# Kernel tuning notes

Hardware: AMD Instinct MI355X
Metric: run time of the kernel (lower is better)

Reference implementation:

```python
import jax, jax.numpy as jnp
import numpy as np

D = 2048      # feature dim (fc1 = Linear(2*2048, 2048))
S = 10240


def setup_inputs() -> dict:
    key = jax.random.key(0)
    ks = jax.random.split(key, 16)
    sc = 0.02
    z = lambda *s: jnp.zeros(s, jnp.float32)
    return {
        "x0": jax.random.normal(ks[0], (1, 1, D), jnp.float32),
        "x1": jax.random.normal(ks[1], (1, S, D), jnp.float32),
        # fc1: Linear(4096, 2048)  (stored input-major for x @ W)
        "W1": jax.random.normal(ks[2], (2 * D, D), jnp.float32) * sc,
        "b1": z(D),
        # fc2: Linear(2048, 1)
        "W2": jax.random.normal(ks[3], (D, 1), jnp.float32) * sc,
        "b2": z(1),
        # LSTM(input=1, hidden=1, bidirectional): per-direction gate params [4] = (i,f,g,o)
        "Wih_f": jax.random.normal(ks[4], (4,), jnp.float32) * 0.5,
        "Whh_f": jax.random.normal(ks[5], (4,), jnp.float32) * 0.5,
        "bih_f": z(4),
        "bhh_f": z(4),
        "Wih_b": jax.random.normal(ks[6], (4,), jnp.float32) * 0.5,
        "Whh_b": jax.random.normal(ks[7], (4,), jnp.float32) * 0.5,
        "bih_b": z(4),
        "bhh_b": z(4),
        # fc3: Linear(10, 1)
        "W3": jax.random.normal(ks[8], (10, 1), jnp.float32) * sc,
        "b3": z(1),
    }


def _lstm_dir(x_seq, Wih, Whh, bih, bhh):
    """Single-direction LSTM, input_size=hidden_size=1, batch=1.
    x_seq: [S] scalars. Returns h sequence [S]. PyTorch gate order (i,f,g,o)."""
    b = bih + bhh

    def step(carry, x):
        h, c = carry
        g = Wih * x + Whh * h + b              # [4]
        i = jax.nn.sigmoid(g[0])
        f = jax.nn.sigmoid(g[1])
        gg = jnp.tanh(g[2])
        o = jax.nn.sigmoid(g[3])
        c = f * c + i * gg
        h = o * jnp.tanh(c)
        return (h, c), h

    h0 = jnp.zeros((), x_seq.dtype)
    c0 = jnp.zeros((), x_seq.dtype)
    _, hs = jax.lax.scan(step, (h0, c0), x_seq)
    return hs


def reference(x0, x1, W1, b1, W2, b2,
              Wih_f, Whh_f, bih_f, bhh_f,
              Wih_b, Whh_b, bih_b, bhh_b,
              W3, b3):
    # similarity: cat(|x0 - x1|, x0 + x1) along features (x0 broadcasts over S)
    sim = jnp.concatenate([jnp.abs(x0 - x1), x0 + x1], axis=2)   # [1, S, 2D]
    h = jax.nn.relu(jnp.einsum('bsf,fd->bsd', sim, W1) + b1)     # [1, S, D]
    # (dropout is identity in eval mode)
    s = jax.nn.sigmoid(jnp.einsum('bsd,do->bso', h, W2) + b2)    # [1, S, 1]
    x_seq = s[0, :, 0]                                           # [S]

    h_f = _lstm_dir(x_seq, Wih_f, Whh_f, bih_f, bhh_f)           # [S]
    h_b = _lstm_dir(x_seq[::-1], Wih_b, Whh_b, bih_b, bhh_b)[::-1]
    out = jnp.stack([h_f, h_b], axis=1)                          # [S, 2] == lstm out [S,1,2]

    grp = out.reshape(1, -1, 10)                                 # [1, S*2/10, 10]
    y = jax.nn.sigmoid(grp @ W3 + b3)                            # [1, S*2/10, 1]
    return y.reshape(1, -1)
```

## Files before the change

kernel.cpp:

```cpp
#include <hip/hip_runtime.h>
#include <hip/hip_bf16.h>

#define DD 2048
#define SS 10240
#define KK 4096

typedef __bf16 bf16x8 __attribute__((ext_vector_type(8)));
typedef float  f32x4  __attribute__((ext_vector_type(4)));

__device__ __forceinline__ unsigned short f2bf_rne(float x) {
    unsigned int u = __float_as_uint(x);
    u += 0x7FFFu + ((u >> 16) & 1u);
    return (unsigned short)(u >> 16);
}

__global__ __launch_bounds__(256) void prep_sim_kernel(
    const float* __restrict__ W1, const float* __restrict__ b2,
    const float* __restrict__ x0, const float* __restrict__ x1,
    unsigned short* __restrict__ W1T, float* __restrict__ s_pre,
    unsigned short* __restrict__ simB) {
    __shared__ float tile[64][65];
    const int t = threadIdx.x;

    if (blockIdx.x < (KK / 64) * (DD / 64)) {
        const int bf = blockIdx.x % (KK / 64);
        const int bd = blockIdx.x / (KK / 64);
        const int f0 = bf * 64, d0 = bd * 64;
#pragma unroll
        for (int p = 0; p < 4; ++p) {
            int fr = p * 16 + (t >> 4);
            int dc = (t & 15) * 4;
            const float4 v = *(const float4*)&W1[(size_t)(f0 + fr) * DD + d0 + dc];
            tile[fr][dc + 0] = v.x; tile[fr][dc + 1] = v.y;
            tile[fr][dc + 2] = v.z; tile[fr][dc + 3] = v.w;
        }
        __syncthreads();
#pragma unroll
        for (int p = 0; p < 4; ++p) {
            int dr = p * 16 + (t >> 4);
            int fc = (t & 15) * 4;
            ushort4 o;
            o.x = f2bf_rne(tile[fc + 0][dr]);
            o.y = f2bf_rne(tile[fc + 1][dr]);
            o.z = f2bf_rne(tile[fc + 2][dr]);
            o.w = f2bf_rne(tile[fc + 3][dr]);
            *(ushort4*)&W1T[(size_t)(d0 + dr) * KK + f0 + fc] = o;
        }
        int gid = blockIdx.x * 256 + t;
        if (gid < SS) s_pre[gid] = b2[0];
    } else {
        const int s = blockIdx.x - (KK / 64) * (DD / 64);
        const int d = t * 8;
        const float4 a0 = *(const float4*)&x0[d];
        const float4 a1 = *(const float4*)&x0[d + 4];
        const float4 v0 = *(const float4*)&x1[(size_t)s * DD + d];
        const float4 v1 = *(const float4*)&x1[(size_t)s * DD + d + 4];
        ushort4 lo0, lo1, hi0, hi1;
        lo0.x = f2bf_rne(fabsf(a0.x - v0.x)); hi0.x = f2bf_rne(a0.x + v0.x);
        lo0.y = f2bf_rne(fabsf(a0.y - v0.y)); hi0.y = f2bf_rne(a0.y + v0.y);
        lo0.z = f2bf_rne(fabsf(a0.z - v0.z)); hi0.z = f2bf_rne(a0.z + v0.z);
        lo0.w = f2bf_rne(fabsf(a0.w - v0.w)); hi0.w = f2bf_rne(a0.w + v0.w);
        lo1.x = f2bf_rne(fabsf(a1.x - v1.x)); hi1.x = f2bf_rne(a1.x + v1.x);
        lo1.y = f2bf_rne(fabsf(a1.y - v1.y)); hi1.y = f2bf_rne(a1.y + v1.y);
        lo1.z = f2bf_rne(fabsf(a1.z - v1.z)); hi1.z = f2bf_rne(a1.z + v1.z);
        lo1.w = f2bf_rne(fabsf(a1.w - v1.w)); hi1.w = f2bf_rne(a1.w + v1.w);
        unsigned short* row = &simB[(size_t)s * KK];
        *(ushort4*)&row[d]          = lo0;
        *(ushort4*)&row[d + 4]      = lo1;
        *(ushort4*)&row[DD + d]     = hi0;
        *(ushort4*)&row[DD + d + 4] = hi1;
    }
}

#define BM3 320
#define BN3 256
#define BK3 64
#define NKT (KK / BK3)

#define STAGE_A(ktv, BUFV)                                                     \
    _Pragma("unroll")                                                          \
    for (int L = 0; L < 5; ++L) {                                              \
        __builtin_amdgcn_global_load_lds(                                      \
            (const __attribute__((address_space(1))) void*)(gA + (size_t)L * 64 * KK + (size_t)(ktv) * 64), \
            (__attribute__((address_space(3))) void*)&lds[BUFV][t * 8 + L * 4096], \
            16, 0, 0);                                                         \
    }
#define STAGE_B(ktv, BUFV)                                                     \
    _Pragma("unroll")                                                          \
    for (int L = 0; L < 4; ++L) {                                              \
        __builtin_amdgcn_global_load_lds(                                      \
            (const __attribute__((address_space(1))) void*)(gB + (size_t)L * 64 * KK + (size_t)(ktv) * 64), \
            (__attribute__((address_space(3))) void*)&lds[BUFV][20480 + t * 8 + L * 4096], \
            16, 0, 0);                                                         \
    }

#define BODY(ktv, BUF, SA_LIT, SB_LIT, DO_STAGE)                               \
    {                                                                          \
        asm volatile("s_waitcnt vmcnt(" SA_LIT ")" ::: "memory");              \
        __builtin_amdgcn_s_barrier();                                          \
        __builtin_amdgcn_sched_barrier(0);                                     \
        if (DO_STAGE) { STAGE_A((ktv) + 1, BUF ^ 1) }                          \
        asm volatile("s_waitcnt vmcnt(" SB_LIT ")" ::: "memory");              \
        __builtin_amdgcn_s_barrier();                                          \
        __builtin_amdgcn_sched_barrier(0);                                     \
        if (DO_STAGE) { STAGE_B((ktv) + 1, BUF ^ 1) }                          \
        _Pragma("unroll")                                                      \
        for (int ks = 0; ks < 2; ++ks) {                                       \
            const int gx = ks ? gx1 : gx0;                                     \
            bf16x8 bfr[8];                                                     \
            _Pragma("unroll")                                                  \
            for (int n = 0; n < 8; ++n)                                        \
                bfr[n] = *(const bf16x8*)&lds[BUF][boff + n * 1024 + gx];      \
            _Pragma("unroll")                                                  \
            for (int m = 0; m < 5; ++m) {                                      \
                bf16x8 afr = *(const bf16x8*)&lds[BUF][aoff + m * 1024 + gx];  \
                __builtin_amdgcn_s_setprio(1);                                 \
                _Pragma("unroll")                                              \
                for (int n = 0; n < 8; ++n)                                    \
                    acc[m][n] = __builtin_amdgcn_mfma_f32_16x16x32_bf16(       \
                        afr, bfr[n], acc[m][n], 0, 0, 0);                      \
                __builtin_amdgcn_s_setprio(0);                                 \
            }                                                                  \
        }                                                                      \
    }

__global__ __launch_bounds__(512, 2) void gemm3_kernel(
    const unsigned short* __restrict__ simB,
    const unsigned short* __restrict__ W1T,
    const float* __restrict__ b1, const float* __restrict__ W2,
    float* __restrict__ s_pre) {
    __shared__ unsigned short lds[2][36864];

    const int t    = threadIdx.x;
    const int lane = t & 63;
    const int wv   = t >> 6;
    const int wr   = wv >> 1;
    const int wc   = wv & 1;
    const int lr   = lane & 15;
    const int g4   = lane >> 4;
    const int l7   = lane & 7;

    const int bm = blockIdx.x & 31;
    const int bn = blockIdx.x >> 5;
    const int m0 = bm * BM3, n0 = bn * BN3;

    const int trow = t >> 3;
    const int gsrc = (t & 7) ^ (trow & 7);
    const unsigned short* gA = simB + (size_t)(m0 + trow) * KK + gsrc * 8;
    const unsigned short* gB = W1T  + (size_t)(n0 + trow) * KK + gsrc * 8;

    const int aoff = (wr * 80 + lr) * 64;
    const int boff = 20480 + (wc * 128 + lr) * 64;
    const int gx0  = ((0 * 4 + g4) ^ l7) * 8;
    const int gx1  = ((1 * 4 + g4) ^ l7) * 8;

    f32x4 acc[5][8];
#pragma unroll
    for (int m = 0; m < 5; ++m)
#pragma unroll
        for (int n = 0; n < 8; ++n)
            acc[m][n] = (f32x4){0.f, 0.f, 0.f, 0.f};

    STAGE_A(0, 0)
    STAGE_B(0, 0)

#pragma unroll 1
    for (int kt = 0; kt < NKT - 2; kt += 2) {
        BODY(kt,     0, "4", "5", 1)
        BODY(kt + 1, 1, "4", "5", 1)
    }
    BODY(NKT - 2, 0, "4", "5", 1)
    BODY(NKT - 1, 1, "4", "0", 0)

    float b1v[8], w2v[8];
#pragma unroll
    for (int n = 0; n < 8; ++n) {
        int col = n0 + wc * 128 + n * 16 + lr;
        b1v[n] = b1[col];
        w2v[n] = W2[col];
    }
#pragma unroll
    for (int m = 0; m < 5; ++m) {
#pragma unroll
        for (int r = 0; r < 4; ++r) {
            float rowsum = 0.f;
#pragma unroll
            for (int n = 0; n < 8; ++n) {
                float v = acc[m][n][r] + b1v[n];
                v = fmaxf(v, 0.f);
                rowsum = fmaf(v, w2v[n], rowsum);
            }
            rowsum += __shfl_xor(rowsum, 1);
            rowsum += __shfl_xor(rowsum, 2);
            rowsum += __shfl_xor(rowsum, 4);
            rowsum += __shfl_xor(rowsum, 8);
            if (lr == 0) {
                int row = m0 + wr * 80 + m * 16 + g4 * 4 + r;
                atomicAdd(&s_pre[row], rowsum);
            }
        }
    }
}

#define BM 128
#define BN 128
#define BK 32

__global__ __launch_bounds__(256) void gemm_kernel(
    const float* __restrict__ x0, const float* __restrict__ x1,
    const unsigned short* __restrict__ W1T,
    const float* __restrict__ b1, const float* __restrict__ W2,
    float* __restrict__ s_pre) {
    __shared__ unsigned short As[BM][BK];
    __shared__ unsigned short Bs[BN][BK];

    const int tid  = threadIdx.x;
    const int lane = tid & 63;
    const int wave = tid >> 6;
    const int wr = wave >> 1, wc = wave & 1;
    const int bm = blockIdx.x / (DD / BN);
    const int bn = blockIdx.x % (DD / BN);
    const int m0 = bm * BM, n0 = bn * BN;
    const int lr = lane & 15;
    const int lk = (lane >> 4) * 8;

    f32x4 acc[4][4];
#pragma unroll
    for (int m = 0; m < 4; ++m)
#pragma unroll
        for (int n = 0; n < 4; ++n)
            acc[m][n] = (f32x4){0.f, 0.f, 0.f, 0.f};

    for (int k0 = 0; k0 < KK; k0 += BK) {
        __syncthreads();
#pragma unroll
        for (int p = 0; p < 2; ++p) {
            int L  = tid + p * 256;
            int n  = L >> 2;
            int k8 = (L & 3) * 8;
            const unsigned short* g = &W1T[(size_t)(n0 + n) * KK + k0 + k8];
            unsigned short* l = &Bs[0][0] + (size_t)L * 8;
            __builtin_amdgcn_global_load_lds(
                (const __attribute__((address_space(1))) void*)g,
                (__attribute__((address_space(3))) void*)l, 16, 0, 0);
        }
        {
            const int f0 = k0 & (DD - 1);
            const bool second = (k0 >= DD);
            const int fc = (tid & 7) * 4;
            const float4 v0 = *(const float4*)&x0[f0 + fc];
#pragma unroll
            for (int p = 0; p < 4; ++p) {
                int row = p * 32 + (tid >> 3);
                const float4 v1 = *(const float4*)&x1[(size_t)(m0 + row) * DD + f0 + fc];
                ushort4 o;
                o.x = f2bf_rne(second ? (v0.x + v1.x) : fabsf(v0.x - v1.x));
                o.y = f2bf_rne(second ? (v0.y + v1.y) : fabsf(v0.y - v1.y));
                o.z = f2bf_rne(second ? (v0.z + v1.z) : fabsf(v0.z - v1.z));
                o.w = f2bf_rne(second ? (v0.w + v1.w) : fabsf(v0.w - v1.w));
                *(ushort4*)&As[row][fc] = o;
            }
        }
        __syncthreads();

        bf16x8 a[4], b[4];
#pragma unroll
        for (int m = 0; m < 4; ++m)
            a[m] = *(const bf16x8*)&As[wr * 64 + m * 16 + lr][lk];
#pragma unroll
        for (int n = 0; n < 4; ++n)
            b[n] = *(const bf16x8*)&Bs[wc * 64 + n * 16 + lr][lk];
#pragma unroll
        for (int m = 0; m < 4; ++m)
#pragma unroll
            for (int n = 0; n < 4; ++n)
                acc[m][n] = __builtin_amdgcn_mfma_f32_16x16x32_bf16(
                    a[m], b[n], acc[m][n], 0, 0, 0);
    }

    float b1v[4], w2v[4];
#pragma unroll
    for (int n = 0; n < 4; ++n) {
        int col = n0 + wc * 64 + n * 16 + lr;
        b1v[n] = b1[col];
        w2v[n] = W2[col];
    }
#pragma unroll
    for (int m = 0; m < 4; ++m) {
#pragma unroll
        for (int r = 0; r < 4; ++r) {
            float rowsum = 0.f;
#pragma unroll
            for (int n = 0; n < 4; ++n) {
                float v = acc[m][n][r] + b1v[n];
                v = fmaxf(v, 0.f);
                rowsum = fmaf(v, w2v[n], rowsum);
            }
            rowsum += __shfl_xor(rowsum, 1);
            rowsum += __shfl_xor(rowsum, 2);
            rowsum += __shfl_xor(rowsum, 4);
            rowsum += __shfl_xor(rowsum, 8);
            if (lr == 0) {
                int row = m0 + wr * 64 + m * 16 + (lane >> 4) * 4 + r;
                atomicAdd(&s_pre[row], rowsum);
            }
        }
    }
}

#define CHUNK 64
#define WARM  192
#define NCH   (SS / CHUNK)

__device__ __forceinline__ float sigf(float x) {
    return 1.f / (1.f + __expf(-x));
}
__device__ __forceinline__ float tanhfast(float x) {
    return 2.f / (1.f + __expf(-2.f * x)) - 1.f;
}

__global__ __launch_bounds__(64) void lstm_kernel(
    const float* __restrict__ s_pre,
    const float* __restrict__ Wih_f, const float* __restrict__ Whh_f,
    const float* __restrict__ bih_f, const float* __restrict__ bhh_f,
    const float* __restrict__ Wih_b, const float* __restrict__ Whh_b,
    const float* __restrict__ bih_b, const float* __restrict__ bhh_b,
    float* __restrict__ hf, float* __restrict__ hb) {
    int id = blockIdx.x * blockDim.x + threadIdx.x;
    if (id >= 2 * NCH) return;
    int dir = id / NCH;
    int ch  = id % NCH;
    const float* Wih = dir ? Wih_b : Wih_f;
    const float* Whh = dir ? Whh_b : Whh_f;
    const float* bih = dir ? bih_b : bih_f;
    const float* bhh = dir ? bhh_b : bhh_f;
    const float wi0 = Wih[0], wi1 = Wih[1], wi2 = Wih[2], wi3 = Wih[3];
    const float wh0 = Whh[0], wh1 = Whh[1], wh2 = Whh[2], wh3 = Whh[3];
    const float bb0 = bih[0] + bhh[0], bb1 = bih[1] + bhh[1];
    const float bb2 = bih[2] + bhh[2], bb3 = bih[3] + bhh[3];

    const int pout0 = ch * CHUNK;
    int pstart = pout0 - WARM; if (pstart < 0) pstart = 0;
    const int pend = pout0 + CHUNK;

    float h = 0.f, c = 0.f;
    for (int p = pstart; p < pend; ++p) {
        int s = dir ? (SS - 1 - p) : p;
        float x  = sigf(s_pre[s]);
        float g0 = fmaf(wi0, x, fmaf(wh0, h, bb0));
        float g1 = fmaf(wi1, x, fmaf(wh1, h, bb1));
        float g2 = fmaf(wi2, x, fmaf(wh2, h, bb2));
        float g3 = fmaf(wi3, x, fmaf(wh3, h, bb3));
        float gi = sigf(g0);
        float gf = sigf(g1);
        float gg = tanhfast(g2);
        float go = sigf(g3);
        c = fmaf(gf, c, gi * gg);
        h = go * tanhfast(c);
        if (p >= pout0) {
            if (dir) hb[s] = h; else hf[s] = h;
        }
    }
}

__global__ __launch_bounds__(256) void final_kernel(
    const float* __restrict__ hf, const float* __restrict__ hb,
    const float* __restrict__ W3, const float* __restrict__ b3,
    float* __restrict__ out) {
    int j = blockIdx.x * blockDim.x + threadIdx.x;
    if (j >= (SS * 2) / 10) return;
    float acc = b3[0];
#pragma unroll
    for (int i = 0; i < 5; ++i) {
        acc = fmaf(hf[5 * j + i], W3[2 * i],     acc);
        acc = fmaf(hb[5 * j + i], W3[2 * i + 1], acc);
    }
    out[j] = sigf(acc);
}

extern "C" void kernel_launch(void* const* d_in, const int* in_sizes, int n_in,
                              void* d_out, int out_size, void* d_ws, size_t ws_size,
                              hipStream_t stream) {
    const float* x0    = (const float*)d_in[0];
    const float* x1    = (const float*)d_in[1];
    const float* W1    = (const float*)d_in[2];
    const float* b1    = (const float*)d_in[3];
    const float* W2    = (const float*)d_in[4];
    const float* b2    = (const float*)d_in[5];
    const float* Wih_f = (const float*)d_in[6];
    const float* Whh_f = (const float*)d_in[7];
    const float* bih_f = (const float*)d_in[8];
    const float* bhh_f = (const float*)d_in[9];
    const float* Wih_b = (const float*)d_in[10];
    const float* Whh_b = (const float*)d_in[11];
    const float* bih_b = (const float*)d_in[12];
    const float* bhh_b = (const float*)d_in[13];
    const float* W3    = (const float*)d_in[14];
    const float* b3    = (const float*)d_in[15];
    float* out = (float*)d_out;

    char* ws = (char*)d_ws;
    const size_t w1t_bytes = (size_t)KK * DD * 2;
    unsigned short* W1T = (unsigned short*)ws;
    float* s_pre = (float*)(ws + w1t_bytes);
    float* hf    = s_pre + SS;
    float* hb    = hf + SS;
    size_t off_sim = w1t_bytes + 3 * (size_t)SS * 4;
    off_sim = (off_sim + 255) & ~(size_t)255;
    unsigned short* simB = (unsigned short*)(ws + off_sim);
    const size_t need = off_sim + (size_t)SS * KK * 2;

    if (ws_size >= need) {
        prep_sim_kernel<<<(KK / 64) * (DD / 64) + SS, 256, 0, stream>>>(
            W1, b2, x0, x1, W1T, s_pre, simB);
        gemm3_kernel<<<(SS / BM3) * (DD / BN3), 512, 0, stream>>>(
            simB, W1T, b1, W2, s_pre);
    } else {
        prep_sim_kernel<<<(KK / 64) * (DD / 64), 256, 0, stream>>>(
            W1, b2, x0, x1, W1T, s_pre, simB);
        gemm_kernel<<<(SS / BM) * (DD / BN), 256, 0, stream>>>(
            x0, x1, W1T, b1, W2, s_pre);
    }
    lstm_kernel<<<(2 * NCH + 63) / 64, 64, 0, stream>>>(
        s_pre, Wih_f, Whh_f, bih_f, bhh_f, Wih_b, Whh_b, bih_b, bhh_b, hf, hb);
    final_kernel<<<((SS * 2) / 10 + 255) / 256, 256, 0, stream>>>(hf, hb, W3, b3, out);
}
```

Baseline: 400.3 us.

## Batch LDS fragment loads into half-tiles in GEMM loop and vectorize LSTM input reads

The GEMM inner loop now loads all A fragments plus half the B fragments at once. It then runs MFMAs on the first four N columns, loads the remaining B fragments, and runs the second half. Barriers and priority raises bracket each MFMA burst to line up the waves and lower register pressure. The LSTM chunk loop reads s_pre as float4 and unrolls four timesteps, which assumes the chunk start and length are multiples of four. The added barriers may stall waves, and the float4 path depends on alignment assumptions.

```diff
diff --git a/kernel.cpp b/kernel.cpp
--- a/kernel.cpp
+++ b/kernel.cpp
@@ -107,20 +107,34 @@
         _Pragma("unroll")                                                      \
         for (int ks = 0; ks < 2; ++ks) {                                       \
             const int gx = ks ? gx1 : gx0;                                     \
-            bf16x8 bfr[8];                                                     \
+            bf16x8 afr[5], bfr[4];                                             \
             _Pragma("unroll")                                                  \
-            for (int n = 0; n < 8; ++n)                                        \
+            for (int m = 0; m < 5; ++m)                                        \
+                afr[m] = *(const bf16x8*)&lds[BUF][aoff + m * 1024 + gx];      \
+            _Pragma("unroll")                                                  \
+            for (int n = 0; n < 4; ++n)                                        \
                 bfr[n] = *(const bf16x8*)&lds[BUF][boff + n * 1024 + gx];      \
+            __builtin_amdgcn_s_barrier();                                      \
+            __builtin_amdgcn_s_setprio(1);                                     \
             _Pragma("unroll")                                                  \
-            for (int m = 0; m < 5; ++m) {                                      \
-                bf16x8 afr = *(const bf16x8*)&lds[BUF][aoff + m * 1024 + gx];  \
-                __builtin_amdgcn_s_setprio(1);                                 \
+            for (int m = 0; m < 5; ++m)                                        \
                 _Pragma("unroll")                                              \
-                for (int n = 0; n < 8; ++n)                                    \
+                for (int n = 0; n < 4; ++n)                                    \
                     acc[m][n] = __builtin_amdgcn_mfma_f32_16x16x32_bf16(       \
-                        afr, bfr[n], acc[m][n], 0, 0, 0);                      \
-                __builtin_amdgcn_s_setprio(0);                                 \
-            }                                                                  \
+                        afr[m], bfr[n], acc[m][n], 0, 0, 0);                   \
+            __builtin_amdgcn_s_setprio(0);                                     \
+            _Pragma("unroll")                                                  \
+            for (int n = 0; n < 4; ++n)                                        \
+                bfr[n] = *(const bf16x8*)&lds[BUF][boff + (4 + n) * 1024 + gx]; \
+            __builtin_amdgcn_s_barrier();                                      \
+            __builtin_amdgcn_s_setprio(1);                                     \
+            _Pragma("unroll")                                                  \
+            for (int m = 0; m < 5; ++m)                                        \
+                _Pragma("unroll")                                              \
+                for (int n = 0; n < 4; ++n)                                    \
+                    acc[m][4 + n] = __builtin_amdgcn_mfma_f32_16x16x32_bf16(   \
+                        afr[m], bfr[n], acc[m][4 + n], 0, 0, 0);               \
+            __builtin_amdgcn_s_setprio(0);                                     \
         }                                                                      \
     }
 
@@ -344,21 +358,34 @@
     const int pend = pout0 + CHUNK;
 
     float h = 0.f, c = 0.f;
-    for (int p = pstart; p < pend; ++p) {
-        int s = dir ? (SS - 1 - p) : p;
-        float x  = sigf(s_pre[s]);
-        float g0 = fmaf(wi0, x, fmaf(wh0, h, bb0));
-        float g1 = fmaf(wi1, x, fmaf(wh1, h, bb1));
-        float g2 = fmaf(wi2, x, fmaf(wh2, h, bb2));
-        float g3 = fmaf(wi3, x, fmaf(wh3, h, bb3));
-        float gi = sigf(g0);
-        float gf = sigf(g1);
-        float gg = tanhfast(g2);
-        float go = sigf(g3);
-        c = fmaf(gf, c, gi * gg);
-        h = go * tanhfast(c);
-        if (p >= pout0) {
-            if (dir) hb[s] = h; else hf[s] = h;
+    for (int p4 = pstart; p4 < pend; p4 += 4) {
+        float4 xv;
+        if (dir == 0) {
+            xv = *(const float4*)&s_pre[p4];
+        } else {
+            const float4 tv = *(const float4*)&s_pre[SS - 4 - p4];
+            xv = (float4){tv.w, tv.z, tv.y, tv.x};
+        }
+        const bool wr_out = (p4 >= pout0);
+        const float xa[4] = {xv.x, xv.y, xv.z, xv.w};
+#pragma unroll
+        for (int q = 0; q < 4; ++q) {
+            const int p = p4 + q;
+            float x  = sigf(xa[q]);
+            float g0 = fmaf(wi0, x, fmaf(wh0, h, bb0));
+            float g1 = fmaf(wi1, x, fmaf(wh1, h, bb1));
+            float g2 = fmaf(wi2, x, fmaf(wh2, h, bb2));
+            float g3 = fmaf(wi3, x, fmaf(wh3, h, bb3));
+            float gi = sigf(g0);
+            float gf = sigf(g1);
+            float gg = tanhfast(g2);
+            float go = sigf(g3);
+            c = fmaf(gf, c, gi * gg);
+            h = go * tanhfast(c);
+            if (wr_out) {
+                int s = dir ? (SS - 1 - p) : p;
+                if (dir) hb[s] = h; else hf[s] = h;
+            }
         }
     }
 }
```

After: 388.4 us. 1.03x faster.
